# Performance work log

Hardware: AMD Instinct MI355X
Metric: run time of the kernel (lower is better)

Reference implementation:

```python
import jax, jax.numpy as jnp
import numpy as np

N_NODES = 100000
N_EDGES = 1600000


def setup_inputs() -> dict:
    key = jax.random.key(0)
    k1, k2, k3, k4 = jax.random.split(key, 4)
    x = jax.random.normal(k1, (N_NODES, 256), dtype=jnp.float32)
    edge_index = jax.random.randint(k2, (2, N_EDGES), 0, N_NODES, dtype=jnp.int64)
    W1 = jax.random.normal(k3, (256, 128), dtype=jnp.float32) * (1.0 / np.sqrt(256))
    W2 = jax.random.normal(k4, (128, 40), dtype=jnp.float32) * (1.0 / np.sqrt(128))
    return {"x": x, "edge_index": edge_index, "W1": W1, "W2": W2}


def _gcn_conv(x, W, src, dst):
    # GCNConv(normalize=False, add_self_loops=False, bias=False):
    # linear transform then sum-aggregate messages along edges src->dst.
    h = x @ W                                   # [N, d_out]
    msg = h[src]                                # [E, d_out] gather
    return jax.ops.segment_sum(msg, dst, num_segments=N_NODES)  # [N, d_out] scatter-add


def reference(x, edge_index, W1, W2):
    src, dst = edge_index[0], edge_index[1]
    h = jax.nn.relu(_gcn_conv(x, W1, src, dst))
    # dropout is identity in eval mode
    out = _gcn_conv(h, W2, src, dst)
    return out
```

## Files before the change

### kernel.cpp

```cpp
#include <hip/hip_runtime.h>

constexpr int NN = 100000;
constexpr int NE = 1600000;
constexpr int DI = 256, DH = 128, DO = 40;

constexpr int NB = (NN + 255) >> 8;
constexpr int NB_BLK = 128;
constexpr int CHUNK = NE / NB_BLK;
constexpr int M2 = NB * NB_BLK;
constexpr int NBS = (M2 + 1023) / 1024;
constexpr int STAGE_CAP = 6144;

typedef __attribute__((ext_vector_type(8))) __bf16 bf16x8;
typedef __attribute__((ext_vector_type(4))) float f32x4;

__device__ inline float bf2f(__bf16 b) { return (float)b; }
__device__ inline float4 bf4_to_f4(ushort4 u) {
    return make_float4(__builtin_bit_cast(float, (unsigned)u.x << 16),
                       __builtin_bit_cast(float, (unsigned)u.y << 16),
                       __builtin_bit_cast(float, (unsigned)u.z << 16),
                       __builtin_bit_cast(float, (unsigned)u.w << 16));
}
__device__ inline unsigned short f2bf(float f) {
    return __builtin_bit_cast(unsigned short, (__bf16)f);
}
__device__ inline bf16x8 bf16x8_zero() {
    bf16x8 r;
    #pragma unroll
    for (int j = 0; j < 8; ++j) r[j] = (__bf16)0.f;
    return r;
}
__device__ inline bf16x8 load_cvt_a(const float* __restrict__ p, bool ok) {
    if (!ok) return bf16x8_zero();
    bf16x8 r;
    const float4 v0 = *(const float4*)p;
    const float4 v1 = *(const float4*)(p + 4);
    r[0] = (__bf16)v0.x; r[1] = (__bf16)v0.y; r[2] = (__bf16)v0.z; r[3] = (__bf16)v0.w;
    r[4] = (__bf16)v1.x; r[5] = (__bf16)v1.y; r[6] = (__bf16)v1.z; r[7] = (__bf16)v1.w;
    return r;
}

__global__ __launch_bounds__(256) void w1pack_kernel(const float* __restrict__ W,
                                                     __bf16* __restrict__ Wf) {
    const int i = blockIdx.x * 256 + threadIdx.x;
    const int j = i & 7;
    const int lane = (i >> 3) & 63;
    const int nt = (i >> 9) & 7;
    const int kt = i >> 12;
    const int k = kt * 32 + (lane >> 4) * 8 + j;
    const int n = nt * 16 + (lane & 15);
    Wf[i] = (__bf16)W[(size_t)k * DH + n];
}

__global__ __launch_bounds__(256) void gemm1_kernel(const float* __restrict__ x,
                                                    const __bf16* __restrict__ Wf,
                                                    __bf16* __restrict__ h1) {
    const int t = threadIdx.x;
    const int wave = t >> 6, lane = t & 63;
    const int q = lane >> 4, m = lane & 15;
    const int row0 = blockIdx.x * 64 + wave * 16;
    const int r = row0 + m;
    const bool ok = r < NN;
    const float* xp = x + (size_t)r * DI;

    bf16x8 a[8];
    #pragma unroll
    for (int kt = 0; kt < 8; ++kt)
        a[kt] = load_cvt_a(xp + kt * 32 + q * 8, ok);

    f32x4 acc[8];
    #pragma unroll
    for (int nt = 0; nt < 8; ++nt)
        #pragma unroll
        for (int rr = 0; rr < 4; ++rr) acc[nt][rr] = 0.f;

    const bf16x8* wf = (const bf16x8*)Wf;
    #pragma unroll
    for (int kt = 0; kt < 8; ++kt) {
        #pragma unroll
        for (int nt = 0; nt < 8; ++nt) {
            const bf16x8 b = wf[(kt * 8 + nt) * 64 + lane];
            acc[nt] = __builtin_amdgcn_mfma_f32_16x16x32_bf16(a[kt], b, acc[nt], 0, 0, 0);
        }
    }
    #pragma unroll
    for (int reg = 0; reg < 4; ++reg) {
        const int rr = row0 + q * 4 + reg;
        if (rr < NN) {
            __bf16* hp = h1 + (size_t)rr * DH + m;
            #pragma unroll
            for (int nt = 0; nt < 8; ++nt) hp[nt * 16] = (__bf16)acc[nt][reg];
        }
    }
}

__global__ __launch_bounds__(256) void bucket_hist_kernel(const int* __restrict__ dst,
                                                          int* __restrict__ hist2d) {
    __shared__ int h[NB];
    for (int i = threadIdx.x; i < NB; i += 256) h[i] = 0;
    __syncthreads();
    const int base = blockIdx.x * CHUNK;
    for (int i = threadIdx.x; i < CHUNK; i += 256)
        atomicAdd(&h[dst[base + i] >> 8], 1);
    __syncthreads();
    for (int i = threadIdx.x; i < NB; i += 256)
        hist2d[i * NB_BLK + blockIdx.x] = h[i];
}

__global__ __launch_bounds__(256) void spart_kernel(const int* __restrict__ in,
                                                    int* __restrict__ bsum) {
    __shared__ int red[256];
    const int idx = blockIdx.x * 1024 + threadIdx.x * 4;
    int s = 0;
    if (idx < M2) { const int4 v = *(const int4*)(in + idx); s = v.x + v.y + v.z + v.w; }
    red[threadIdx.x] = s;
    __syncthreads();
    #pragma unroll
    for (int d = 128; d > 0; d >>= 1) {
        if (threadIdx.x < d) red[threadIdx.x] += red[threadIdx.x + d];
        __syncthreads();
    }
    if (threadIdx.x == 0) bsum[blockIdx.x] = red[0];
}

__global__ __launch_bounds__(64) void sblock_kernel(const int* __restrict__ bsum,
                                                    int* __restrict__ boff) {
    __shared__ int part[64];
    const int t = threadIdx.x;
    const int v = (t < NBS) ? bsum[t] : 0;
    part[t] = v;
    __syncthreads();
    for (int d = 1; d < 64; d <<= 1) {
        const int u = (t >= d) ? part[t - d] : 0;
        __syncthreads();
        part[t] += u;
        __syncthreads();
    }
    if (t < NBS) boff[t] = part[t] - v;
}

__global__ __launch_bounds__(256) void sfinal_kernel(const int* __restrict__ in,
                                                     const int* __restrict__ boff,
                                                     int* __restrict__ out) {
    __shared__ int part[256];
    const int t = threadIdx.x;
    const int idx = blockIdx.x * 1024 + t * 4;
    int4 v = make_int4(0, 0, 0, 0);
    if (idx < M2) v = *(const int4*)(in + idx);
    const int s = v.x + v.y + v.z + v.w;
    part[t] = s;
    __syncthreads();
    for (int d = 1; d < 256; d <<= 1) {
        const int u = (t >= d) ? part[t - d] : 0;
        __syncthreads();
        part[t] += u;
        __syncthreads();
    }
    if (idx < M2) {
        const int base = boff[blockIdx.x] + part[t] - s;
        *(int4*)(out + idx) = make_int4(base, base + v.x, base + v.x + v.y,
                                        base + v.x + v.y + v.z);
    }
}

__global__ __launch_bounds__(256) void bucket_scatter_kernel(const int* __restrict__ src,
                                                             const int* __restrict__ dst,
                                                             const int* __restrict__ offs2d,
                                                             unsigned* __restrict__ epack) {
    __shared__ int cur[NB];
    for (int i = threadIdx.x; i < NB; i += 256)
        cur[i] = offs2d[i * NB_BLK + blockIdx.x];
    __syncthreads();
    const int base = blockIdx.x * CHUNK;
    for (int i = threadIdx.x; i < CHUNK; i += 256) {
        const int d = dst[base + i], s = src[base + i];
        const int p = atomicAdd(&cur[d >> 8], 1);
        epack[p] = (unsigned)s | ((unsigned)(d & 255) << 24);
    }
}

__global__ __launch_bounds__(256) void bucket_sort_kernel(const unsigned* __restrict__ epack,
                                                          const int* __restrict__ offs2d,
                                                          int* __restrict__ off,
                                                          int* __restrict__ esrc) {
    __shared__ int cnt[256];
    __shared__ int incl[256];
    __shared__ int cur[256];
    __shared__ int stage[STAGE_CAP];
    const int b = blockIdx.x;
    const int t = threadIdx.x;
    const int bstart = offs2d[b * NB_BLK];
    const int bend = (b + 1 < NB) ? offs2d[(b + 1) * NB_BLK] : NE;
    const int n = bend - bstart;
    cnt[t] = 0;
    __syncthreads();
    for (int i = t; i < n; i += 256)
        atomicAdd(&cnt[epack[bstart + i] >> 24], 1);
    __syncthreads();
    incl[t] = cnt[t];
    __syncthreads();
    for (int d = 1; d < 256; d <<= 1) {
        const int u = (t >= d) ? incl[t - d] : 0;
        __syncthreads();
        incl[t] += u;
        __syncthreads();
    }
    const int ex = incl[t] - cnt[t];
    const int node = (b << 8) + t;
    if (node <= NN) off[node] = bstart + ex;
    cur[t] = ex;
    __syncthreads();
    const bool staged = (n <= STAGE_CAP);
    for (int i = t; i < n; i += 256) {
        const unsigned pk = epack[bstart + i];
        const int p = atomicAdd(&cur[pk >> 24], 1);
        const int s = (int)(pk & 0xFFFFFFu);
        if (staged) stage[p] = s;
        else esrc[bstart + p] = s;
    }
    __syncthreads();
    if (staged)
        for (int i = t; i < n; i += 256) esrc[bstart + i] = stage[i];
}

__global__ __launch_bounds__(256) void agg1_kernel(const __bf16* __restrict__ h1,
                                                   const int* __restrict__ esrc,
                                                   const int* __restrict__ off,
                                                   __bf16* __restrict__ agg) {
    const int w = (blockIdx.x * 256 + threadIdx.x) >> 6;
    if (w >= NN) return;
    const int lane = threadIdx.x & 63;
    const int half = lane >> 5;
    const int c = (lane & 31) * 4;
    const int b = off[w], e = off[w + 1];
    float4 a0 = make_float4(0.f, 0.f, 0.f, 0.f);
    float4 a1 = a0, a2 = a0, a3 = a0;
    int j = b + half;
    for (; j + 6 < e; j += 8) {
        const int s0 = esrc[j], s1 = esrc[j + 2], s2 = esrc[j + 4], s3 = esrc[j + 6];
        const float4 v0 = bf4_to_f4(*(const ushort4*)(h1 + (size_t)s0 * DH + c));
        const float4 v1 = bf4_to_f4(*(const ushort4*)(h1 + (size_t)s1 * DH + c));
        const float4 v2 = bf4_to_f4(*(const ushort4*)(h1 + (size_t)s2 * DH + c));
        const float4 v3 = bf4_to_f4(*(const ushort4*)(h1 + (size_t)s3 * DH + c));
        a0.x += v0.x; a0.y += v0.y; a0.z += v0.z; a0.w += v0.w;
        a1.x += v1.x; a1.y += v1.y; a1.z += v1.z; a1.w += v1.w;
        a2.x += v2.x; a2.y += v2.y; a2.z += v2.z; a2.w += v2.w;
        a3.x += v3.x; a3.y += v3.y; a3.z += v3.z; a3.w += v3.w;
    }
    for (; j < e; j += 2) {
        const int s = esrc[j];
        const float4 v = bf4_to_f4(*(const ushort4*)(h1 + (size_t)s * DH + c));
        a0.x += v.x; a0.y += v.y; a0.z += v.z; a0.w += v.w;
    }
    float4 acc = make_float4(a0.x + a1.x + a2.x + a3.x,
                             a0.y + a1.y + a2.y + a3.y,
                             a0.z + a1.z + a2.z + a3.z,
                             a0.w + a1.w + a2.w + a3.w);
    acc.x += __shfl_xor(acc.x, 32);
    acc.y += __shfl_xor(acc.y, 32);
    acc.z += __shfl_xor(acc.z, 32);
    acc.w += __shfl_xor(acc.w, 32);
    if (half == 0) {
        ushort4 o;
        o.x = f2bf(fmaxf(acc.x, 0.f));
        o.y = f2bf(fmaxf(acc.y, 0.f));
        o.z = f2bf(fmaxf(acc.z, 0.f));
        o.w = f2bf(fmaxf(acc.w, 0.f));
        *(ushort4*)(agg + (size_t)w * DH + c) = o;
    }
}

__global__ __launch_bounds__(256) void gemm2_kernel(const __bf16* __restrict__ agg,
                                                    const float* __restrict__ W2,
                                                    __bf16* __restrict__ h2) {
    __shared__ __bf16 Wt2[48][136];
    const int t = threadIdx.x;
    const int wave = t >> 6, lane = t & 63;
    const int q = lane >> 4, m = lane & 15;
    const int row0 = blockIdx.x * 64 + wave * 16;
    for (int i = t; i < DH * DO; i += 256) {
        const int k = i / DO, n = i % DO;
        Wt2[n][k] = (__bf16)W2[i];
    }
    for (int i = t; i < 8 * DH; i += 256)
        Wt2[DO + (i >> 7)][i & 127] = (__bf16)0.f;
    __syncthreads();
    const int r = row0 + m;
    const bool okA = r < NN;
    const __bf16* ap = agg + (size_t)r * DH;
    f32x4 acc[3];
    #pragma unroll
    for (int nt = 0; nt < 3; ++nt)
        #pragma unroll
        for (int rr = 0; rr < 4; ++rr) acc[nt][rr] = 0.f;
    #pragma unroll
    for (int ks = 0; ks < 4; ++ks) {
        const int k0 = ks * 32 + q * 8;
        const bf16x8 a = okA ? *(const bf16x8*)(ap + k0) : bf16x8_zero();
        #pragma unroll
        for (int nt = 0; nt < 3; ++nt) {
            const bf16x8 b = *(const bf16x8*)(&Wt2[nt * 16 + m][k0]);
            acc[nt] = __builtin_amdgcn_mfma_f32_16x16x32_bf16(a, b, acc[nt], 0, 0, 0);
        }
    }
    #pragma unroll
    for (int reg = 0; reg < 4; ++reg) {
        const int rr = row0 + q * 4 + reg;
        if (rr < NN) {
            #pragma unroll
            for (int nt = 0; nt < 3; ++nt) {
                const int cc = nt * 16 + m;
                if (cc < DO) h2[(size_t)rr * DO + cc] = (__bf16)acc[nt][reg];
            }
        }
    }
}

__global__ __launch_bounds__(256) void agg2_kernel(const __bf16* __restrict__ h2,
                                                   const int* __restrict__ esrc,
                                                   const int* __restrict__ off,
                                                   float* __restrict__ out) {
    const int w = (blockIdx.x * 256 + threadIdx.x) >> 6;
    if (w >= NN) return;
    const int lane = threadIdx.x & 63;
    const int sub = lane / 10;
    const int c = (lane % 10) * 4;
    const int b = off[w], e = off[w + 1];
    float4 a0 = make_float4(0.f, 0.f, 0.f, 0.f);
    float4 a1 = a0, a2 = a0;
    if (sub < 6) {
        int j = b + sub;
        for (; j + 12 < e; j += 18) {
            const int s0 = esrc[j], s1 = esrc[j + 6], s2 = esrc[j + 12];
            const float4 v0 = bf4_to_f4(*(const ushort4*)(h2 + (size_t)s0 * DO + c));
            const float4 v1 = bf4_to_f4(*(const ushort4*)(h2 + (size_t)s1 * DO + c));
            const float4 v2 = bf4_to_f4(*(const ushort4*)(h2 + (size_t)s2 * DO + c));
            a0.x += v0.x; a0.y += v0.y; a0.z += v0.z; a0.w += v0.w;
            a1.x += v1.x; a1.y += v1.y; a1.z += v1.z; a1.w += v1.w;
            a2.x += v2.x; a2.y += v2.y; a2.z += v2.z; a2.w += v2.w;
        }
        for (; j < e; j += 6) {
            const int s = esrc[j];
            const float4 v = bf4_to_f4(*(const ushort4*)(h2 + (size_t)s * DO + c));
            a0.x += v.x; a0.y += v.y; a0.z += v.z; a0.w += v.w;
        }
    }
    float4 acc = make_float4(a0.x + a1.x + a2.x, a0.y + a1.y + a2.y,
                             a0.z + a1.z + a2.z, a0.w + a1.w + a2.w);
    acc.x += __shfl(acc.x, lane + 30);
    acc.y += __shfl(acc.y, lane + 30);
    acc.z += __shfl(acc.z, lane + 30);
    acc.w += __shfl(acc.w, lane + 30);
    const float ax = acc.x + __shfl(acc.x, lane + 10) + __shfl(acc.x, lane + 20);
    const float ay = acc.y + __shfl(acc.y, lane + 10) + __shfl(acc.y, lane + 20);
    const float az = acc.z + __shfl(acc.z, lane + 10) + __shfl(acc.z, lane + 20);
    const float aw = acc.w + __shfl(acc.w, lane + 10) + __shfl(acc.w, lane + 20);
    if (lane < 10) {
        *(float4*)(out + (size_t)w * DO + c) = make_float4(ax, ay, az, aw);
    }
}

extern "C" void kernel_launch(void* const* d_in, const int* in_sizes, int n_in,
                              void* d_out, int out_size, void* d_ws, size_t ws_size,
                              hipStream_t stream) {
    const float* x  = (const float*)d_in[0];
    const int*   ei = (const int*)d_in[1];
    const float* W1 = (const float*)d_in[2];
    const float* W2 = (const float*)d_in[3];
    const int* src = ei;
    const int* dst = ei + NE;

    __bf16* Wf  = (__bf16*)d_ws;
    __bf16* h1  = Wf + 32768;
    __bf16* agg = h1 + (size_t)NN * DH;
    __bf16* h2  = h1;
    unsigned* epack = (unsigned*)(agg + (size_t)NN * DH);
    int* ints   = (int*)(epack + NE);
    int* esrc   = ints;
    int* off    = esrc + NE;
    int* hist2d = off + NN + 1;
    int* offs2d = hist2d + M2;
    int* bsum   = offs2d + M2;
    int* boff   = bsum + NBS;

    float* out = (float*)d_out;

    w1pack_kernel<<<128, 256, 0, stream>>>(W1, Wf);
    gemm1_kernel<<<(NN + 63) / 64, 256, 0, stream>>>(x, Wf, h1);
    bucket_hist_kernel<<<NB_BLK, 256, 0, stream>>>(dst, hist2d);
    spart_kernel<<<NBS, 256, 0, stream>>>(hist2d, bsum);
    sblock_kernel<<<1, 64, 0, stream>>>(bsum, boff);
    sfinal_kernel<<<NBS, 256, 0, stream>>>(hist2d, boff, offs2d);
    bucket_scatter_kernel<<<NB_BLK, 256, 0, stream>>>(src, dst, offs2d, epack);
    bucket_sort_kernel<<<NB, 256, 0, stream>>>(epack, offs2d, off, esrc);
    agg1_kernel<<<(NN * 64 + 255) / 256, 256, 0, stream>>>(h1, esrc, off, agg);
    gemm2_kernel<<<(NN + 63) / 64, 256, 0, stream>>>(agg, W2, h2);
    agg2_kernel<<<(NN * 64 + 255) / 256, 256, 0, stream>>>(h2, esrc, off, out);
}
```

Before: 366.7 us.

## Fuse layer-1 aggregation with second GEMM via shared-memory row tiles

Merges the first-layer gather/sum and the second GEMM into one kernel. Each wave aggregates 16 nodes into an LDS tile and then runs MFMA against W2, which is pre-packed into fragment order by a new small kernel. This drops the global round trip of the 100k x 128 bf16 aggregate and one launch. The cost is far fewer waves in flight for the gather-heavy part: one wave now loops serially over 16 nodes instead of one wave per node, so latency hiding may get worse. It also widens the layer-1 unroll to 8 and narrows the agg2 unroll to 2.

```diff
diff --git a/kernel.cpp b/kernel.cpp
--- a/kernel.cpp
+++ b/kernel.cpp
@@ -14,7 +14,6 @@
 typedef __attribute__((ext_vector_type(8))) __bf16 bf16x8;
 typedef __attribute__((ext_vector_type(4))) float f32x4;
 
-__device__ inline float bf2f(__bf16 b) { return (float)b; }
 __device__ inline float4 bf4_to_f4(ushort4 u) {
     return make_float4(__builtin_bit_cast(float, (unsigned)u.x << 16),
                        __builtin_bit_cast(float, (unsigned)u.y << 16),
@@ -50,6 +49,18 @@
     const int k = kt * 32 + (lane >> 4) * 8 + j;
     const int n = nt * 16 + (lane & 15);
     Wf[i] = (__bf16)W[(size_t)k * DH + n];
+}
+
+__global__ __launch_bounds__(256) void w2pack_kernel(const float* __restrict__ W2,
+                                                     __bf16* __restrict__ Wf2) {
+    const int i = blockIdx.x * 256 + threadIdx.x;
+    const int j = i & 7;
+    const int lane = (i >> 3) & 63;
+    const int g = i >> 9;
+    const int nt = g % 3, ks = g / 3;
+    const int k = ks * 32 + (lane >> 4) * 8 + j;
+    const int n = nt * 16 + (lane & 15);
+    Wf2[i] = (n < DO) ? (__bf16)W2[(size_t)k * DO + n] : (__bf16)0.f;
 }
 
 __global__ __launch_bounds__(256) void gemm1_kernel(const float* __restrict__ x,
@@ -223,94 +234,95 @@
         for (int i = t; i < n; i += 256) esrc[bstart + i] = stage[i];
 }
 
-__global__ __launch_bounds__(256) void agg1_kernel(const __bf16* __restrict__ h1,
-                                                   const int* __restrict__ esrc,
-                                                   const int* __restrict__ off,
-                                                   __bf16* __restrict__ agg) {
-    const int w = (blockIdx.x * 256 + threadIdx.x) >> 6;
-    if (w >= NN) return;
-    const int lane = threadIdx.x & 63;
+__global__ __launch_bounds__(256) void agg1g2_kernel(const __bf16* __restrict__ h1,
+                                                     const int* __restrict__ esrc,
+                                                     const int* __restrict__ off,
+                                                     const __bf16* __restrict__ Wf2,
+                                                     __bf16* __restrict__ h2) {
+    __shared__ __bf16 rows[4][16][136];
+    const int t = threadIdx.x;
+    const int wave = t >> 6, lane = t & 63;
     const int half = lane >> 5;
     const int c = (lane & 31) * 4;
-    const int b = off[w], e = off[w + 1];
-    float4 a0 = make_float4(0.f, 0.f, 0.f, 0.f);
-    float4 a1 = a0, a2 = a0, a3 = a0;
-    int j = b + half;
-    for (; j + 6 < e; j += 8) {
-        const int s0 = esrc[j], s1 = esrc[j + 2], s2 = esrc[j + 4], s3 = esrc[j + 6];
-        const float4 v0 = bf4_to_f4(*(const ushort4*)(h1 + (size_t)s0 * DH + c));
-        const float4 v1 = bf4_to_f4(*(const ushort4*)(h1 + (size_t)s1 * DH + c));
-        const float4 v2 = bf4_to_f4(*(const ushort4*)(h1 + (size_t)s2 * DH + c));
-        const float4 v3 = bf4_to_f4(*(const ushort4*)(h1 + (size_t)s3 * DH + c));
-        a0.x += v0.x; a0.y += v0.y; a0.z += v0.z; a0.w += v0.w;
-        a1.x += v1.x; a1.y += v1.y; a1.z += v1.z; a1.w += v1.w;
-        a2.x += v2.x; a2.y += v2.y; a2.z += v2.z; a2.w += v2.w;
-        a3.x += v3.x; a3.y += v3.y; a3.z += v3.z; a3.w += v3.w;
-    }
-    for (; j < e; j += 2) {
-        const int s = esrc[j];
-        const float4 v = bf4_to_f4(*(const ushort4*)(h1 + (size_t)s * DH + c));
-        a0.x += v.x; a0.y += v.y; a0.z += v.z; a0.w += v.w;
-    }
-    float4 acc = make_float4(a0.x + a1.x + a2.x + a3.x,
-                             a0.y + a1.y + a2.y + a3.y,
-                             a0.z + a1.z + a2.z + a3.z,
-                             a0.w + a1.w + a2.w + a3.w);
-    acc.x += __shfl_xor(acc.x, 32);
-    acc.y += __shfl_xor(acc.y, 32);
-    acc.z += __shfl_xor(acc.z, 32);
-    acc.w += __shfl_xor(acc.w, 32);
-    if (half == 0) {
-        ushort4 o;
-        o.x = f2bf(fmaxf(acc.x, 0.f));
-        o.y = f2bf(fmaxf(acc.y, 0.f));
-        o.z = f2bf(fmaxf(acc.z, 0.f));
-        o.w = f2bf(fmaxf(acc.w, 0.f));
-        *(ushort4*)(agg + (size_t)w * DH + c) = o;
-    }
-}
-
-__global__ __launch_bounds__(256) void gemm2_kernel(const __bf16* __restrict__ agg,
-                                                    const float* __restrict__ W2,
-                                                    __bf16* __restrict__ h2) {
-    __shared__ __bf16 Wt2[48][136];
-    const int t = threadIdx.x;
-    const int wave = t >> 6, lane = t & 63;
     const int q = lane >> 4, m = lane & 15;
-    const int row0 = blockIdx.x * 64 + wave * 16;
-    for (int i = t; i < DH * DO; i += 256) {
-        const int k = i / DO, n = i % DO;
-        Wt2[n][k] = (__bf16)W2[i];
-    }
-    for (int i = t; i < 8 * DH; i += 256)
-        Wt2[DO + (i >> 7)][i & 127] = (__bf16)0.f;
-    __syncthreads();
-    const int r = row0 + m;
-    const bool okA = r < NN;
-    const __bf16* ap = agg + (size_t)r * DH;
-    f32x4 acc[3];
+    const int node0 = blockIdx.x * 64 + wave * 16;
+
+    for (int i = 0; i < 16; ++i) {
+        const int n = node0 + i;
+        float4 a0 = make_float4(0.f, 0.f, 0.f, 0.f);
+        float4 a1 = a0, a2 = a0, a3 = a0, a4 = a0, a5 = a0, a6 = a0, a7 = a0;
+        if (n < NN) {
+            const int b = off[n], e = off[n + 1];
+            int j = b + half;
+            for (; j + 14 < e; j += 16) {
+                const int s0 = esrc[j],      s1 = esrc[j + 2],  s2 = esrc[j + 4],  s3 = esrc[j + 6];
+                const int s4 = esrc[j + 8],  s5 = esrc[j + 10], s6 = esrc[j + 12], s7 = esrc[j + 14];
+                const float4 v0 = bf4_to_f4(*(const ushort4*)(h1 + (size_t)s0 * DH + c));
+                const float4 v1 = bf4_to_f4(*(const ushort4*)(h1 + (size_t)s1 * DH + c));
+                const float4 v2 = bf4_to_f4(*(const ushort4*)(h1 + (size_t)s2 * DH + c));
+                const float4 v3 = bf4_to_f4(*(const ushort4*)(h1 + (size_t)s3 * DH + c));
+                const float4 v4 = bf4_to_f4(*(const ushort4*)(h1 + (size_t)s4 * DH + c));
+                const float4 v5 = bf4_to_f4(*(const ushort4*)(h1 + (size_t)s5 * DH + c));
+                const float4 v6 = bf4_to_f4(*(const ushort4*)(h1 + (size_t)s6 * DH + c));
+                const float4 v7 = bf4_to_f4(*(const ushort4*)(h1 + (size_t)s7 * DH + c));
+                a0.x += v0.x; a0.y += v0.y; a0.z += v0.z; a0.w += v0.w;
+                a1.x += v1.x; a1.y += v1.y; a1.z += v1.z; a1.w += v1.w;
+                a2.x += v2.x; a2.y += v2.y; a2.z += v2.z; a2.w += v2.w;
+                a3.x += v3.x; a3.y += v3.y; a3.z += v3.z; a3.w += v3.w;
+                a4.x += v4.x; a4.y += v4.y; a4.z += v4.z; a4.w += v4.w;
+                a5.x += v5.x; a5.y += v5.y; a5.z += v5.z; a5.w += v5.w;
+                a6.x += v6.x; a6.y += v6.y; a6.z += v6.z; a6.w += v6.w;
+                a7.x += v7.x; a7.y += v7.y; a7.z += v7.z; a7.w += v7.w;
+            }
+            for (; j < e; j += 2) {
+                const int s = esrc[j];
+                const float4 v = bf4_to_f4(*(const ushort4*)(h1 + (size_t)s * DH + c));
+                a0.x += v.x; a0.y += v.y; a0.z += v.z; a0.w += v.w;
+            }
+        }
+        float4 acc = make_float4(a0.x + a1.x + a2.x + a3.x + a4.x + a5.x + a6.x + a7.x,
+                                 a0.y + a1.y + a2.y + a3.y + a4.y + a5.y + a6.y + a7.y,
+                                 a0.z + a1.z + a2.z + a3.z + a4.z + a5.z + a6.z + a7.z,
+                                 a0.w + a1.w + a2.w + a3.w + a4.w + a5.w + a6.w + a7.w);
+        acc.x += __shfl_xor(acc.x, 32);
+        acc.y += __shfl_xor(acc.y, 32);
+        acc.z += __shfl_xor(acc.z, 32);
+        acc.w += __shfl_xor(acc.w, 32);
+        if (half == 0) {
+            ushort4 o;
+            o.x = f2bf(fmaxf(acc.x, 0.f));
+            o.y = f2bf(fmaxf(acc.y, 0.f));
+            o.z = f2bf(fmaxf(acc.z, 0.f));
+            o.w = f2bf(fmaxf(acc.w, 0.f));
+            *(ushort4*)(&rows[wave][i][c]) = o;
+        }
+    }
+    __syncthreads();
+
+    f32x4 acc2[3];
     #pragma unroll
     for (int nt = 0; nt < 3; ++nt)
         #pragma unroll
-        for (int rr = 0; rr < 4; ++rr) acc[nt][rr] = 0.f;
+        for (int rr = 0; rr < 4; ++rr) acc2[nt][rr] = 0.f;
+    const bf16x8* wf2 = (const bf16x8*)Wf2;
     #pragma unroll
     for (int ks = 0; ks < 4; ++ks) {
         const int k0 = ks * 32 + q * 8;
-        const bf16x8 a = okA ? *(const bf16x8*)(ap + k0) : bf16x8_zero();
+        const bf16x8 a = *(const bf16x8*)(&rows[wave][m][k0]);
         #pragma unroll
         for (int nt = 0; nt < 3; ++nt) {
-            const bf16x8 b = *(const bf16x8*)(&Wt2[nt * 16 + m][k0]);
-            acc[nt] = __builtin_amdgcn_mfma_f32_16x16x32_bf16(a, b, acc[nt], 0, 0, 0);
+            const bf16x8 b = wf2[(ks * 3 + nt) * 64 + lane];
+            acc2[nt] = __builtin_amdgcn_mfma_f32_16x16x32_bf16(a, b, acc2[nt], 0, 0, 0);
         }
     }
     #pragma unroll
     for (int reg = 0; reg < 4; ++reg) {
-        const int rr = row0 + q * 4 + reg;
+        const int rr = node0 + q * 4 + reg;
         if (rr < NN) {
             #pragma unroll
             for (int nt = 0; nt < 3; ++nt) {
                 const int cc = nt * 16 + m;
-                if (cc < DO) h2[(size_t)rr * DO + cc] = (__bf16)acc[nt][reg];
+                if (cc < DO) h2[(size_t)rr * DO + cc] = (__bf16)acc2[nt][reg];
             }
         }
     }
@@ -327,17 +339,15 @@
     const int c = (lane % 10) * 4;
     const int b = off[w], e = off[w + 1];
     float4 a0 = make_float4(0.f, 0.f, 0.f, 0.f);
-    float4 a1 = a0, a2 = a0;
+    float4 a1 = a0;
     if (sub < 6) {
         int j = b + sub;
-        for (; j + 12 < e; j += 18) {
-            const int s0 = esrc[j], s1 = esrc[j + 6], s2 = esrc[j + 12];
+        for (; j + 6 < e; j += 12) {
+            const int s0 = esrc[j], s1 = esrc[j + 6];
             const float4 v0 = bf4_to_f4(*(const ushort4*)(h2 + (size_t)s0 * DO + c));
             const float4 v1 = bf4_to_f4(*(const ushort4*)(h2 + (size_t)s1 * DO + c));
-            const float4 v2 = bf4_to_f4(*(const ushort4*)(h2 + (size_t)s2 * DO + c));
             a0.x += v0.x; a0.y += v0.y; a0.z += v0.z; a0.w += v0.w;
             a1.x += v1.x; a1.y += v1.y; a1.z += v1.z; a1.w += v1.w;
-            a2.x += v2.x; a2.y += v2.y; a2.z += v2.z; a2.w += v2.w;
         }
         for (; j < e; j += 6) {
             const int s = esrc[j];
@@ -345,8 +355,7 @@
             a0.x += v.x; a0.y += v.y; a0.z += v.z; a0.w += v.w;
         }
     }
-    float4 acc = make_float4(a0.x + a1.x + a2.x, a0.y + a1.y + a2.y,
-                             a0.z + a1.z + a2.z, a0.w + a1.w + a2.w);
+    float4 acc = make_float4(a0.x + a1.x, a0.y + a1.y, a0.z + a1.z, a0.w + a1.w);
     acc.x += __shfl(acc.x, lane + 30);
     acc.y += __shfl(acc.y, lane + 30);
     acc.z += __shfl(acc.z, lane + 30);
@@ -371,12 +380,11 @@
     const int* dst = ei + NE;
 
     __bf16* Wf  = (__bf16*)d_ws;
-    __bf16* h1  = Wf + 32768;
-    __bf16* agg = h1 + (size_t)NN * DH;
-    __bf16* h2  = h1;
-    unsigned* epack = (unsigned*)(agg + (size_t)NN * DH);
-    int* ints   = (int*)(epack + NE);
-    int* esrc   = ints;
+    __bf16* Wf2 = Wf + 32768;
+    __bf16* h1  = Wf2 + 6144;
+    __bf16* h2  = h1 + (size_t)NN * DH;
+    unsigned* epack = (unsigned*)(h2 + (size_t)NN * DO);
+    int* esrc   = (int*)(epack + NE);
     int* off    = esrc + NE;
     int* hist2d = off + NN + 1;
     int* offs2d = hist2d + M2;
@@ -386,6 +394,7 @@
     float* out = (float*)d_out;
 
     w1pack_kernel<<<128, 256, 0, stream>>>(W1, Wf);
+    w2pack_kernel<<<24, 256, 0, stream>>>(W2, Wf2);
     gemm1_kernel<<<(NN + 63) / 64, 256, 0, stream>>>(x, Wf, h1);
     bucket_hist_kernel<<<NB_BLK, 256, 0, stream>>>(dst, hist2d);
     spart_kernel<<<NBS, 256, 0, stream>>>(hist2d, bsum);
@@ -393,7 +402,6 @@
     sfinal_kernel<<<NBS, 256, 0, stream>>>(hist2d, boff, offs2d);
     bucket_scatter_kernel<<<NB_BLK, 256, 0, stream>>>(src, dst, offs2d, epack);
     bucket_sort_kernel<<<NB, 256, 0, stream>>>(epack, offs2d, off, esrc);
-    agg1_kernel<<<(NN * 64 + 255) / 256, 256, 0, stream>>>(h1, esrc, off, agg);
-    gemm2_kernel<<<(NN + 63) / 64, 256, 0, stream>>>(agg, W2, h2);
+    agg1g2_kernel<<<(NN + 63) / 64, 256, 0, stream>>>(h1, esrc, off, Wf2, h2);
     agg2_kernel<<<(NN * 64 + 255) / 256, 256, 0, stream>>>(h2, esrc, off, out);
 }
```

New measurement: 421.1 us. 14.8% more time.

## Cooperatively load edge indices with shuffles in aggregation and prepack W2 fragments

Applied to the files above, without the earlier changes.

In both aggregation kernels, each wave now reads up to 64 neighbour indices in one coalesced load and hands them to lanes with __shfl. This replaces the old scalar per-lane index loads and raises unrolling to more independent gathers in flight (8 in agg1, 4 in agg2). W2 is packed once into MFMA B-fragment order by the combined pack kernel, so every gemm2 block no longer converts it into shared memory and waits on a barrier. The cost is more shuffle instructions and more registers per lane, which may lower occupancy.

```diff
diff --git a/kernel.cpp b/kernel.cpp
--- a/kernel.cpp
+++ b/kernel.cpp
@@ -14,7 +14,6 @@
 typedef __attribute__((ext_vector_type(8))) __bf16 bf16x8;
 typedef __attribute__((ext_vector_type(4))) float f32x4;
 
-__device__ inline float bf2f(__bf16 b) { return (float)b; }
 __device__ inline float4 bf4_to_f4(ushort4 u) {
     return make_float4(__builtin_bit_cast(float, (unsigned)u.x << 16),
                        __builtin_bit_cast(float, (unsigned)u.y << 16),
@@ -39,17 +38,35 @@
     r[4] = (__bf16)v1.x; r[5] = (__bf16)v1.y; r[6] = (__bf16)v1.z; r[7] = (__bf16)v1.w;
     return r;
 }
-
-__global__ __launch_bounds__(256) void w1pack_kernel(const float* __restrict__ W,
-                                                     __bf16* __restrict__ Wf) {
-    const int i = blockIdx.x * 256 + threadIdx.x;
-    const int j = i & 7;
-    const int lane = (i >> 3) & 63;
-    const int nt = (i >> 9) & 7;
-    const int kt = i >> 12;
-    const int k = kt * 32 + (lane >> 4) * 8 + j;
-    const int n = nt * 16 + (lane & 15);
-    Wf[i] = (__bf16)W[(size_t)k * DH + n];
+__device__ inline void acc4(float4& a, float4 v) {
+    a.x += v.x; a.y += v.y; a.z += v.z; a.w += v.w;
+}
+
+__global__ __launch_bounds__(256) void wpack_kernel(const float* __restrict__ W1,
+                                                    const float* __restrict__ W2,
+                                                    __bf16* __restrict__ Wf,
+                                                    __bf16* __restrict__ Wf2) {
+    if (blockIdx.x < 128) {
+        const int i = blockIdx.x * 256 + threadIdx.x;
+        const int j = i & 7;
+        const int lane = (i >> 3) & 63;
+        const int nt = (i >> 9) & 7;
+        const int kt = i >> 12;
+        const int k = kt * 32 + (lane >> 4) * 8 + j;
+        const int n = nt * 16 + (lane & 15);
+        Wf[i] = (__bf16)W1[(size_t)k * DH + n];
+    } else {
+        const int i = (blockIdx.x - 128) * 256 + threadIdx.x;
+        if (i < 6144) {
+            const int j = i & 7;
+            const int lane = (i >> 3) & 63;
+            const int g = i >> 9;
+            const int nt = g % 3, ks = g / 3;
+            const int k = ks * 32 + (lane >> 4) * 8 + j;
+            const int n = nt * 16 + (lane & 15);
+            Wf2[i] = (n < DO) ? (__bf16)W2[(size_t)k * DO + n] : (__bf16)0.f;
+        }
+    }
 }
 
 __global__ __launch_bounds__(256) void gemm1_kernel(const float* __restrict__ x,
@@ -233,29 +250,54 @@
     const int half = lane >> 5;
     const int c = (lane & 31) * 4;
     const int b = off[w], e = off[w + 1];
+    const int deg = e - b;
     float4 a0 = make_float4(0.f, 0.f, 0.f, 0.f);
-    float4 a1 = a0, a2 = a0, a3 = a0;
-    int j = b + half;
-    for (; j + 6 < e; j += 8) {
-        const int s0 = esrc[j], s1 = esrc[j + 2], s2 = esrc[j + 4], s3 = esrc[j + 6];
-        const float4 v0 = bf4_to_f4(*(const ushort4*)(h1 + (size_t)s0 * DH + c));
-        const float4 v1 = bf4_to_f4(*(const ushort4*)(h1 + (size_t)s1 * DH + c));
-        const float4 v2 = bf4_to_f4(*(const ushort4*)(h1 + (size_t)s2 * DH + c));
-        const float4 v3 = bf4_to_f4(*(const ushort4*)(h1 + (size_t)s3 * DH + c));
-        a0.x += v0.x; a0.y += v0.y; a0.z += v0.z; a0.w += v0.w;
-        a1.x += v1.x; a1.y += v1.y; a1.z += v1.z; a1.w += v1.w;
-        a2.x += v2.x; a2.y += v2.y; a2.z += v2.z; a2.w += v2.w;
-        a3.x += v3.x; a3.y += v3.y; a3.z += v3.z; a3.w += v3.w;
-    }
-    for (; j < e; j += 2) {
-        const int s = esrc[j];
-        const float4 v = bf4_to_f4(*(const ushort4*)(h1 + (size_t)s * DH + c));
-        a0.x += v.x; a0.y += v.y; a0.z += v.z; a0.w += v.w;
-    }
-    float4 acc = make_float4(a0.x + a1.x + a2.x + a3.x,
-                             a0.y + a1.y + a2.y + a3.y,
-                             a0.z + a1.z + a2.z + a3.z,
-                             a0.w + a1.w + a2.w + a3.w);
+    float4 a1 = a0, a2 = a0, a3 = a0, a4 = a0, a5 = a0, a6 = a0, a7 = a0;
+
+    for (int base = 0; base < deg; base += 64) {
+        const int cnt = min(64, deg - base);
+        const int cl = cnt - 1;
+        const int idx = (base + lane < deg) ? esrc[b + base + lane] : 0;
+        int kk = 0;
+        for (; kk + 16 <= cnt; kk += 16) {
+            const int s0 = __shfl(idx, kk + half);
+            const int s1 = __shfl(idx, kk + 2 + half);
+            const int s2 = __shfl(idx, kk + 4 + half);
+            const int s3 = __shfl(idx, kk + 6 + half);
+            const int s4 = __shfl(idx, kk + 8 + half);
+            const int s5 = __shfl(idx, kk + 10 + half);
+            const int s6 = __shfl(idx, kk + 12 + half);
+            const int s7 = __shfl(idx, kk + 14 + half);
+            acc4(a0, bf4_to_f4(*(const ushort4*)(h1 + (size_t)s0 * DH + c)));
+            acc4(a1, bf4_to_f4(*(const ushort4*)(h1 + (size_t)s1 * DH + c)));
+            acc4(a2, bf4_to_f4(*(const ushort4*)(h1 + (size_t)s2 * DH + c)));
+            acc4(a3, bf4_to_f4(*(const ushort4*)(h1 + (size_t)s3 * DH + c)));
+            acc4(a4, bf4_to_f4(*(const ushort4*)(h1 + (size_t)s4 * DH + c)));
+            acc4(a5, bf4_to_f4(*(const ushort4*)(h1 + (size_t)s5 * DH + c)));
+            acc4(a6, bf4_to_f4(*(const ushort4*)(h1 + (size_t)s6 * DH + c)));
+            acc4(a7, bf4_to_f4(*(const ushort4*)(h1 + (size_t)s7 * DH + c)));
+        }
+        for (; kk + 8 <= cnt; kk += 8) {
+            const int s0 = __shfl(idx, kk + half);
+            const int s1 = __shfl(idx, kk + 2 + half);
+            const int s2 = __shfl(idx, kk + 4 + half);
+            const int s3 = __shfl(idx, kk + 6 + half);
+            acc4(a0, bf4_to_f4(*(const ushort4*)(h1 + (size_t)s0 * DH + c)));
+            acc4(a1, bf4_to_f4(*(const ushort4*)(h1 + (size_t)s1 * DH + c)));
+            acc4(a2, bf4_to_f4(*(const ushort4*)(h1 + (size_t)s2 * DH + c)));
+            acc4(a3, bf4_to_f4(*(const ushort4*)(h1 + (size_t)s3 * DH + c)));
+        }
+        for (; kk < cnt; kk += 2) {
+            const int ei = kk + half;
+            const int s0 = __shfl(idx, (ei < cnt) ? ei : cl);
+            const float4 v = bf4_to_f4(*(const ushort4*)(h1 + (size_t)s0 * DH + c));
+            if (ei < cnt) acc4(a0, v);
+        }
+    }
+    float4 acc = make_float4(a0.x + a1.x + a2.x + a3.x + a4.x + a5.x + a6.x + a7.x,
+                             a0.y + a1.y + a2.y + a3.y + a4.y + a5.y + a6.y + a7.y,
+                             a0.z + a1.z + a2.z + a3.z + a4.z + a5.z + a6.z + a7.z,
+                             a0.w + a1.w + a2.w + a3.w + a4.w + a5.w + a6.w + a7.w);
     acc.x += __shfl_xor(acc.x, 32);
     acc.y += __shfl_xor(acc.y, 32);
     acc.z += __shfl_xor(acc.z, 32);
@@ -271,35 +313,30 @@
 }
 
 __global__ __launch_bounds__(256) void gemm2_kernel(const __bf16* __restrict__ agg,
-                                                    const float* __restrict__ W2,
+                                                    const __bf16* __restrict__ Wf2,
                                                     __bf16* __restrict__ h2) {
-    __shared__ __bf16 Wt2[48][136];
     const int t = threadIdx.x;
     const int wave = t >> 6, lane = t & 63;
     const int q = lane >> 4, m = lane & 15;
     const int row0 = blockIdx.x * 64 + wave * 16;
-    for (int i = t; i < DH * DO; i += 256) {
-        const int k = i / DO, n = i % DO;
-        Wt2[n][k] = (__bf16)W2[i];
-    }
-    for (int i = t; i < 8 * DH; i += 256)
-        Wt2[DO + (i >> 7)][i & 127] = (__bf16)0.f;
-    __syncthreads();
     const int r = row0 + m;
-    const bool okA = r < NN;
+    const bool ok = r < NN;
     const __bf16* ap = agg + (size_t)r * DH;
+
     f32x4 acc[3];
     #pragma unroll
     for (int nt = 0; nt < 3; ++nt)
         #pragma unroll
         for (int rr = 0; rr < 4; ++rr) acc[nt][rr] = 0.f;
+
+    const bf16x8* wf2 = (const bf16x8*)Wf2;
     #pragma unroll
     for (int ks = 0; ks < 4; ++ks) {
         const int k0 = ks * 32 + q * 8;
-        const bf16x8 a = okA ? *(const bf16x8*)(ap + k0) : bf16x8_zero();
+        const bf16x8 a = ok ? *(const bf16x8*)(ap + k0) : bf16x8_zero();
         #pragma unroll
         for (int nt = 0; nt < 3; ++nt) {
-            const bf16x8 b = *(const bf16x8*)(&Wt2[nt * 16 + m][k0]);
+            const bf16x8 b = wf2[(ks * 3 + nt) * 64 + lane];
             acc[nt] = __builtin_amdgcn_mfma_f32_16x16x32_bf16(a, b, acc[nt], 0, 0, 0);
         }
     }
@@ -326,27 +363,45 @@
     const int sub = lane / 10;
     const int c = (lane % 10) * 4;
     const int b = off[w], e = off[w + 1];
+    const int deg = e - b;
     float4 a0 = make_float4(0.f, 0.f, 0.f, 0.f);
-    float4 a1 = a0, a2 = a0;
-    if (sub < 6) {
-        int j = b + sub;
-        for (; j + 12 < e; j += 18) {
-            const int s0 = esrc[j], s1 = esrc[j + 6], s2 = esrc[j + 12];
+    float4 a1 = a0, a2 = a0, a3 = a0;
+
+    for (int base = 0; base < deg; base += 64) {
+        const int cnt = min(64, deg - base);
+        const int cl = cnt - 1;
+        const int idx = (base + lane < deg) ? esrc[b + base + lane] : 0;
+        const bool act = sub < 6;
+        int kk = 0;
+        for (; kk + 24 <= cnt; kk += 24) {
+            const int e0 = kk + sub;
+            const int s0 = __shfl(idx, min(e0, cl));
+            const int s1 = __shfl(idx, min(e0 + 6, cl));
+            const int s2 = __shfl(idx, min(e0 + 12, cl));
+            const int s3 = __shfl(idx, min(e0 + 18, cl));
             const float4 v0 = bf4_to_f4(*(const ushort4*)(h2 + (size_t)s0 * DO + c));
             const float4 v1 = bf4_to_f4(*(const ushort4*)(h2 + (size_t)s1 * DO + c));
             const float4 v2 = bf4_to_f4(*(const ushort4*)(h2 + (size_t)s2 * DO + c));
-            a0.x += v0.x; a0.y += v0.y; a0.z += v0.z; a0.w += v0.w;
-            a1.x += v1.x; a1.y += v1.y; a1.z += v1.z; a1.w += v1.w;
-            a2.x += v2.x; a2.y += v2.y; a2.z += v2.z; a2.w += v2.w;
-        }
-        for (; j < e; j += 6) {
-            const int s = esrc[j];
-            const float4 v = bf4_to_f4(*(const ushort4*)(h2 + (size_t)s * DO + c));
-            a0.x += v.x; a0.y += v.y; a0.z += v.z; a0.w += v.w;
-        }
-    }
-    float4 acc = make_float4(a0.x + a1.x + a2.x, a0.y + a1.y + a2.y,
-                             a0.z + a1.z + a2.z, a0.w + a1.w + a2.w);
+            const float4 v3 = bf4_to_f4(*(const ushort4*)(h2 + (size_t)s3 * DO + c));
+            if (act) { acc4(a0, v0); acc4(a1, v1); acc4(a2, v2); acc4(a3, v3); }
+        }
+        for (; kk + 12 <= cnt; kk += 12) {
+            const int e0 = kk + sub;
+            const int s0 = __shfl(idx, min(e0, cl));
+            const int s1 = __shfl(idx, min(e0 + 6, cl));
+            const float4 v0 = bf4_to_f4(*(const ushort4*)(h2 + (size_t)s0 * DO + c));
+            const float4 v1 = bf4_to_f4(*(const ushort4*)(h2 + (size_t)s1 * DO + c));
+            if (act) { acc4(a0, v0); acc4(a1, v1); }
+        }
+        for (; kk < cnt; kk += 6) {
+            const int e0 = kk + sub;
+            const int s0 = __shfl(idx, min(e0, cl));
+            const float4 v = bf4_to_f4(*(const ushort4*)(h2 + (size_t)s0 * DO + c));
+            if (act && e0 < cnt) acc4(a0, v);
+        }
+    }
+    float4 acc = make_float4(a0.x + a1.x + a2.x + a3.x, a0.y + a1.y + a2.y + a3.y,
+                             a0.z + a1.z + a2.z + a3.z, a0.w + a1.w + a2.w + a3.w);
     acc.x += __shfl(acc.x, lane + 30);
     acc.y += __shfl(acc.y, lane + 30);
     acc.z += __shfl(acc.z, lane + 30);
@@ -371,12 +426,12 @@
     const int* dst = ei + NE;
 
     __bf16* Wf  = (__bf16*)d_ws;
-    __bf16* h1  = Wf + 32768;
+    __bf16* Wf2 = Wf + 32768;
+    __bf16* h1  = Wf2 + 6144;
     __bf16* agg = h1 + (size_t)NN * DH;
     __bf16* h2  = h1;
     unsigned* epack = (unsigned*)(agg + (size_t)NN * DH);
-    int* ints   = (int*)(epack + NE);
-    int* esrc   = ints;
+    int* esrc   = (int*)(epack + NE);
     int* off    = esrc + NE;
     int* hist2d = off + NN + 1;
     int* offs2d = hist2d + M2;
@@ -385,7 +440,7 @@
 
     float* out = (float*)d_out;
 
-    w1pack_kernel<<<128, 256, 0, stream>>>(W1, Wf);
+    wpack_kernel<<<152, 256, 0, stream>>>(W1, W2, Wf, Wf2);
     gemm1_kernel<<<(NN + 63) / 64, 256, 0, stream>>>(x, Wf, h1);
     bucket_hist_kernel<<<NB_BLK, 256, 0, stream>>>(dst, hist2d);
     spart_kernel<<<NBS, 256, 0, stream>>>(hist2d, bsum);
@@ -394,6 +449,6 @@
     bucket_scatter_kernel<<<NB_BLK, 256, 0, stream>>>(src, dst, offs2d, epack);
     bucket_sort_kernel<<<NB, 256, 0, stream>>>(epack, offs2d, off, esrc);
     agg1_kernel<<<(NN * 64 + 255) / 256, 256, 0, stream>>>(h1, esrc, off, agg);
-    gemm2_kernel<<<(NN + 63) / 64, 256, 0, stream>>>(agg, W2, h2);
+    gemm2_kernel<<<(NN + 63) / 64, 256, 0, stream>>>(agg, Wf2, h2);
     agg2_kernel<<<(NN * 64 + 255) / 256, 256, 0, stream>>>(h2, esrc, off, out);
 }
```

Measured after the change: 366.9 us. About the same (+0.1%).
